# Optimization experiments

Hardware: AMD Instinct MI355X
Metric: run time of the kernel (lower is better)

The kernel has to match this reference:

```python
import jax, jax.numpy as jnp
import numpy as np

EMBED = 512
HEADS = 8
HD = EMBED // HEADS  # 64
LAYERS = 4
VOCAB = 16
SDIM = 3
TDEPTH = 8
BATCH = 2
SEQ = 1024
FF = 4 * EMBED
EPS = 1e-6      # fast-transformers CausalLinearAttention eps
LN_EPS = 1e-5   # torch LayerNorm default


def layer_norm(x, g, b):
    m = jnp.mean(x, axis=-1, keepdims=True)
    v = jnp.mean((x - m) ** 2, axis=-1, keepdims=True)
    return (x - m) * jax.lax.rsqrt(v + LN_EPS) * g + b


def setup_inputs() -> dict:
    key = jax.random.key(0)
    ks = iter(jax.random.split(key, 64))
    def nrm(shape, scale=0.02):
        return jax.random.normal(next(ks), shape, jnp.float32) * scale
    inp = {}
    inp['value'] = jax.random.randint(next(ks), (BATCH, SEQ), 0, VOCAB + 1)
    inp['depth'] = jax.random.randint(next(ks), (BATCH, SEQ), 0, TDEPTH + 1)
    inp['pos'] = jax.random.randint(next(ks), (SDIM, BATCH, SEQ), 0, 2 ** TDEPTH + 1)
    inp['sos'] = jax.random.normal(next(ks), (EMBED,), jnp.float32)
    # embeddings with padding_idx=0 -> zero row 0
    inp['tok_emb'] = nrm((VOCAB + 1, EMBED), 1.0).at[0].set(0.0)
    inp['depth_emb'] = nrm((TDEPTH + 1, EMBED), 1.0).at[0].set(0.0)
    inp['spatial_emb'] = nrm((SDIM, 2 ** TDEPTH + 1, EMBED), 1.0).at[:, 0].set(0.0)
    # per-layer stacked params (weights stored [in, out])
    for nm in ('Wq', 'Wk', 'Wv', 'Wo'):
        inp[nm] = nrm((LAYERS, EMBED, EMBED))
    for nm in ('bq', 'bk', 'bv', 'bo'):
        inp[nm] = jnp.zeros((LAYERS, EMBED), jnp.float32)
    inp['ln1_g'] = jnp.ones((LAYERS, EMBED), jnp.float32)
    inp['ln1_b'] = jnp.zeros((LAYERS, EMBED), jnp.float32)
    inp['ln2_g'] = jnp.ones((LAYERS, EMBED), jnp.float32)
    inp['ln2_b'] = jnp.zeros((LAYERS, EMBED), jnp.float32)
    inp['W1'] = nrm((LAYERS, EMBED, FF))
    inp['b1'] = jnp.zeros((LAYERS, FF), jnp.float32)
    inp['W2'] = nrm((LAYERS, FF, EMBED))
    inp['b2'] = jnp.zeros((LAYERS, EMBED), jnp.float32)
    inp['lnf_g'] = jnp.ones((EMBED,), jnp.float32)
    inp['lnf_b'] = jnp.zeros((EMBED,), jnp.float32)
    inp['Wh'] = nrm((EMBED, VOCAB + 1))
    return inp


def reference(value, depth, pos, sos, tok_emb, depth_emb, spatial_emb,
              Wq, bq, Wk, bk, Wv, bv, Wo, bo,
              ln1_g, ln1_b, ln2_g, ln2_b, W1, b1, W2, b2,
              lnf_g, lnf_b, Wh):
    N, S = value.shape
    # embedding sum
    x = tok_emb[value] + depth_emb[depth]
    for a in range(SDIM):
        x = x + spatial_emb[a][pos[a]]
    # shift right, prepend SOS
    x = jnp.concatenate([jnp.broadcast_to(sos, (N, 1, EMBED)), x[:, :-1, :]], axis=1)
    kmask = (value != 0).astype(x.dtype)  # (N,S) length mask applied to keys
    for i in range(LAYERS):
        # causal-linear attention (elu+1 feature map)
        q = jax.nn.elu((x @ Wq[i] + bq[i]).reshape(N, S, HEADS, HD)) + 1.0
        k = jax.nn.elu((x @ Wk[i] + bk[i]).reshape(N, S, HEADS, HD)) + 1.0
        v = (x @ Wv[i] + bv[i]).reshape(N, S, HEADS, HD)
        k = k * kmask[:, :, None, None]
        kv = jnp.cumsum(jnp.einsum('nshd,nshm->nshdm', k, v), axis=1)  # prefix K^T V state
        num = jnp.einsum('nshd,nshdm->nshm', q, kv)
        z = 1.0 / (jnp.einsum('nshd,nshd->nsh', q, jnp.cumsum(k, axis=1)) + EPS)
        attn = (num * z[..., None]).reshape(N, S, EMBED) @ Wo[i] + bo[i]
        # post-norm transformer block (fast-transformers TransformerEncoderLayer)
        x = layer_norm(x + attn, ln1_g[i], ln1_b[i])
        y = jax.nn.gelu(x @ W1[i] + b1[i], approximate=False) @ W2[i] + b2[i]
        x = layer_norm(x + y, ln2_g[i], ln2_b[i])
    x = layer_norm(x, lnf_g, lnf_b)  # encoder final norm
    return x @ Wh  # (N, S, num_vocab+1)
```

## Files before the change

### kernel.cpp

```cpp
#include <hip/hip_runtime.h>
#include <math.h>

#define EMB 512
#define SEQL 1024
#define NBATCH 2
#define NHEAD 8
#define FFDIM 2048
#define NLAYER 4
#define NROWS (NBATCH*SEQL)
#define CHUNK 128
#define NCH (SEQL/CHUNK)
#define QSTR 1536
#define LN_EPS_F 1e-5f
#define ATT_EPS_F 1e-6f

typedef __bf16 bf16x8 __attribute__((ext_vector_type(8)));
typedef float f32x4 __attribute__((ext_vector_type(4)));

__device__ __forceinline__ unsigned short f2bf(float f) {
    unsigned int u = __float_as_uint(f);
    u += 0x7FFFu + ((u >> 16) & 1u);
    return (unsigned short)(u >> 16);
}
__device__ __forceinline__ float bf2f(unsigned short x) {
    return __uint_as_float(((unsigned int)x) << 16);
}
__device__ __forceinline__ void gl_lds16(const unsigned short* g, unsigned short* l) {
    __builtin_amdgcn_global_load_lds(
        (__attribute__((address_space(1))) void*)const_cast<unsigned short*>(g),
        (__attribute__((address_space(3))) void*)l, 16, 0, 0);
}

__global__ void k_embed(const int* __restrict__ value, const int* __restrict__ depth,
                        const int* __restrict__ pos, const float* __restrict__ sos,
                        const float* __restrict__ tok, const float* __restrict__ dep,
                        const float* __restrict__ spa, float* __restrict__ X,
                        unsigned short* __restrict__ Xb) {
    int row = blockIdx.x;
    int n = row / SEQL, s = row % SEQL;
    int e = threadIdx.x * 4;
    float4 o;
    if (s == 0) {
        o = *(const float4*)(sos + e);
    } else {
        int sp = s - 1;
        int tv = value[n*SEQL + sp];
        int dv = depth[n*SEQL + sp];
        float4 a = *(const float4*)(tok + (size_t)tv*EMB + e);
        float4 b = *(const float4*)(dep + (size_t)dv*EMB + e);
        o.x = a.x+b.x; o.y = a.y+b.y; o.z = a.z+b.z; o.w = a.w+b.w;
#pragma unroll
        for (int ax = 0; ax < 3; ++ax) {
            int p = pos[((size_t)ax*NBATCH + n)*SEQL + sp];
            float4 c = *(const float4*)(spa + ((size_t)ax*257 + p)*EMB + e);
            o.x += c.x; o.y += c.y; o.z += c.z; o.w += c.w;
        }
    }
    *(float4*)(X + (size_t)row*EMB + e) = o;
    ushort4 ob; ob.x = f2bf(o.x); ob.y = f2bf(o.y); ob.z = f2bf(o.z); ob.w = f2bf(o.w);
    *(ushort4*)(Xb + (size_t)row*EMB + e) = ob;
}

__global__ __launch_bounds__(256) void k_wconv(
        const float* __restrict__ Wq0, const float* __restrict__ Wk0, const float* __restrict__ Wv0,
        const float* __restrict__ Wo0, const float* __restrict__ W10, const float* __restrict__ W20,
        const float* __restrict__ bq0, const float* __restrict__ bk0, const float* __restrict__ bv0,
        unsigned short* __restrict__ wAll, float* __restrict__ bqkv) {
    int idx = blockIdx.x*256 + threadIdx.x;
    if (idx >= 1572864) {
        int t = idx - 1572864;
        if (t < 6144) {
            int L = t / 1536, c = t % 1536;
            float v = (c < 512) ? bq0[L*512 + c] : (c < 1024) ? bk0[L*512 + c - 512] : bv0[L*512 + c - 1024];
            bqkv[L*1536 + c] = v;
        }
        return;
    }
    int L = idx / 393216;
    int t0 = idx % 393216;
    const float* Wq = Wq0 + (size_t)L*EMB*EMB;
    const float* Wk = Wk0 + (size_t)L*EMB*EMB;
    const float* Wv = Wv0 + (size_t)L*EMB*EMB;
    const float* Wo = Wo0 + (size_t)L*EMB*EMB;
    const float* W1 = W10 + (size_t)L*EMB*FFDIM;
    const float* W2 = W20 + (size_t)L*FFDIM*EMB;
    unsigned short* lay = wAll + (size_t)L*3145728;
    unsigned short* qkvT = lay;
    unsigned short* woT  = lay + 786432;
    unsigned short* w1T  = lay + 1048576;
    unsigned short* w2T  = lay + 2097152;

    const float* src; unsigned short* dst; size_t soff; size_t doff;
    if (t0 < 131072) {
        int sub = t0 >> 15, t = t0 & 32767;
        int kb = t >> 9, n = t & 511;
        src = (sub == 0) ? Wq : (sub == 1) ? Wk : (sub == 2) ? Wv : Wo;
        soff = (size_t)kb*8*512 + n;
        if (sub < 3) { dst = qkvT; doff = ((size_t)kb*1536 + sub*512 + n)*8; }
        else         { dst = woT;  doff = ((size_t)kb*512 + n)*8; }
        unsigned int p[4];
#pragma unroll
        for (int t2 = 0; t2 < 4; ++t2) {
            unsigned int lo = f2bf(src[soff + (size_t)(2*t2)*512]);
            unsigned int hi = f2bf(src[soff + (size_t)(2*t2+1)*512]);
            p[t2] = lo | (hi << 16);
        }
        *(uint4*)(dst + doff) = make_uint4(p[0], p[1], p[2], p[3]);
    } else if (t0 < 262144) {
        int t = t0 - 131072;
        int kb = t >> 11, n = t & 2047;
        soff = (size_t)kb*8*2048 + n;
        doff = ((size_t)kb*2048 + n)*8;
        unsigned int p[4];
#pragma unroll
        for (int t2 = 0; t2 < 4; ++t2) {
            unsigned int lo = f2bf(W1[soff + (size_t)(2*t2)*2048]);
            unsigned int hi = f2bf(W1[soff + (size_t)(2*t2+1)*2048]);
            p[t2] = lo | (hi << 16);
        }
        *(uint4*)(w1T + doff) = make_uint4(p[0], p[1], p[2], p[3]);
    } else {
        int t = t0 - 262144;
        int kb = t >> 9, n = t & 511;
        soff = (size_t)kb*8*512 + n;
        doff = ((size_t)kb*512 + n)*8;
        unsigned int p[4];
#pragma unroll
        for (int t2 = 0; t2 < 4; ++t2) {
            unsigned int lo = f2bf(W2[soff + (size_t)(2*t2)*512]);
            unsigned int hi = f2bf(W2[soff + (size_t)(2*t2+1)*512]);
            p[t2] = lo | (hi << 16);
        }
        *(uint4*)(w2T + doff) = make_uint4(p[0], p[1], p[2], p[3]);
    }
}

template<int BM, int BN, int WR, int WC, int ACT>
__global__ __launch_bounds__(WR*WC*64) void k_mgemm(
        const unsigned short* __restrict__ A, const unsigned short* __restrict__ Wt,
        const float* __restrict__ bias, const int* __restrict__ maskv,
        float* __restrict__ Cf, unsigned short* __restrict__ Cb,
        int N, int K, int lda, int ldc) {
    constexpr int THREADS = WR*WC*64;
    constexpr int WM = BM/WR, WN = BN/WC;
    constexpr int FM = WM/16, FN = WN/16;
    __shared__ __align__(16) unsigned short As[BM*32];
    __shared__ __align__(16) unsigned short Bs[BN*32];
    int tid = threadIdx.x;
    int lane = tid & 63;
    int l15 = lane & 15, lg = lane >> 4;
    int wid = tid >> 6;
    int wm = (wid / WC) * WM, wn = (wid % WC) * WN;
    int bm = blockIdx.y * BM, bn = blockIdx.x * BN;

    f32x4 acc[FM][FN] = {};

    int a_off = (wm + l15)*32 + lg*8;
    int b_off = lg*BN*8 + (wn + l15)*8;

    for (int k0 = 0; k0 < K; k0 += 32) {
#pragma unroll
        for (int i = 0; i < BM*4/THREADS; ++i) {
            int s = tid + i*THREADS;
            int m = s >> 2, kq = s & 3;
            gl_lds16(A + (size_t)(bm + m)*lda + k0 + kq*8, &As[s*8]);
        }
#pragma unroll
        for (int i = 0; i < BN*4/THREADS; ++i) {
            int s = tid + i*THREADS;
            int kb = s / BN, n = s - kb*BN;
            gl_lds16(Wt + ((size_t)(k0/8 + kb)*N + bn + n)*8, &Bs[s*8]);
        }
        __syncthreads();
        bf16x8 af[FM], bfr[FN];
#pragma unroll
        for (int mi = 0; mi < FM; ++mi) af[mi] = *(const bf16x8*)&As[a_off + mi*512];
#pragma unroll
        for (int ni = 0; ni < FN; ++ni) bfr[ni] = *(const bf16x8*)&Bs[b_off + ni*128];
#pragma unroll
        for (int mi = 0; mi < FM; ++mi)
#pragma unroll
            for (int ni = 0; ni < FN; ++ni)
                acc[mi][ni] = __builtin_amdgcn_mfma_f32_16x16x32_bf16(af[mi], bfr[ni], acc[mi][ni], 0, 0, 0);
        __syncthreads();
    }

    int r0 = bm + wm + lg*4;
    int c0 = bn + wn + l15;
#pragma unroll
    for (int mi = 0; mi < FM; ++mi) {
#pragma unroll
        for (int ni = 0; ni < FN; ++ni) {
            int col = c0 + ni*16;
#pragma unroll
            for (int j = 0; j < 4; ++j) {
                int row = r0 + mi*16 + j;
                float c = acc[mi][ni][j] + bias[col];
                if (ACT == 4) {
                    int reg = col >> 9;
                    if (reg == 0) { c = (c > 0.f) ? c + 1.f : expf(c); }
                    else if (reg == 1) { c = (c > 0.f) ? c + 1.f : expf(c); c *= (maskv[row] != 0) ? 1.f : 0.f; }
                    Cb[(size_t)row*ldc + col] = f2bf(c);
                } else if (ACT == 3) {
                    c = 0.5f * c * (1.f + erff(c * 0.70710678118654752f));
                    Cb[(size_t)row*ldc + col] = f2bf(c);
                } else {
                    Cf[(size_t)row*ldc + col] = c;
                }
            }
        }
    }
}

__global__ __launch_bounds__(256) void k_cpart(
        const unsigned short* __restrict__ QKVb, float* __restrict__ Mpart, float* __restrict__ Upart) {
    int b = blockIdx.x;
    int c = b % NCH, h = (b / NCH) % NHEAD, n = b / (NCH * NHEAD);
    const unsigned short* Kp = QKVb + (size_t)(n*SEQL + c*CHUNK)*QSTR + 512 + h*64;
    const unsigned short* Vp = Kp + 512;
    __shared__ float Ks[8][64], Vs[8][64];
    int tid = threadIdx.x;
    int dk = tid >> 2, dv0 = (tid & 3) * 16;
    int lr = tid >> 5, lc = (tid & 31) * 2;
    float acc[16] = {};
    float uacc = 0.f;
    for (int s0 = 0; s0 < CHUNK; s0 += 8) {
        ushort2 k2 = *(const ushort2*)(Kp + (size_t)(s0 + lr)*QSTR + lc);
        ushort2 v2 = *(const ushort2*)(Vp + (size_t)(s0 + lr)*QSTR + lc);
        Ks[lr][lc] = bf2f(k2.x); Ks[lr][lc+1] = bf2f(k2.y);
        Vs[lr][lc] = bf2f(v2.x); Vs[lr][lc+1] = bf2f(v2.y);
        __syncthreads();
#pragma unroll
        for (int ss = 0; ss < 8; ++ss) {
            float kk = Ks[ss][dk];
#pragma unroll
            for (int j = 0; j < 16; ++j) acc[j] += kk * Vs[ss][dv0 + j];
        }
        if (tid < 64) {
#pragma unroll
            for (int ss = 0; ss < 8; ++ss) uacc += Ks[ss][tid];
        }
        __syncthreads();
    }
    size_t base = ((size_t)(n*NHEAD + h)*NCH + c) * 4096;
#pragma unroll
    for (int j = 0; j < 16; ++j) Mpart[base + (size_t)dk*64 + dv0 + j] = acc[j];
    if (tid < 64) Upart[((size_t)(n*NHEAD + h)*NCH + c)*64 + tid] = uacc;
}

__global__ __launch_bounds__(512) void k_cattend(
        const unsigned short* __restrict__ QKVb, const float* __restrict__ Mpart,
        const float* __restrict__ Upart, unsigned short* __restrict__ Ab) {
    int b = blockIdx.x;
    int c = b % NCH, h = (b / NCH) % NHEAD, n = b / (NCH * NHEAD);
    int nh = n*NHEAD + h;
    int tid = threadIdx.x;
    int wid = tid >> 6, lane = tid & 63;
    int l15 = lane & 15, lg = lane >> 4;
    __shared__ __align__(16) unsigned short Vt[64*200];
    __shared__ __align__(16) unsigned short St[11264];
    __shared__ float wf[64];
    int rowbase = n*SEQL + c*CHUNK;

    {
        int j = tid & 127, vd0 = (tid >> 7) * 16;
        const unsigned short* vp = QKVb + (size_t)(rowbase + j)*QSTR + 1024 + h*64 + vd0;
        uint4 u0 = *(const uint4*)vp;
        uint4 u1 = *(const uint4*)(vp + 8);
        const unsigned short* e0 = (const unsigned short*)&u0;
        const unsigned short* e1 = (const unsigned short*)&u1;
#pragma unroll
        for (int t = 0; t < 8; ++t) Vt[(vd0 + t)*200 + j] = e0[t];
#pragma unroll
        for (int t = 0; t < 8; ++t) Vt[(vd0 + 8 + t)*200 + j] = e1[t];
    }
    {
        int d = tid & 63, vd0 = (tid >> 6) * 8;
        float pr[8] = {};
        for (int cc = 0; cc < c; ++cc) {
            const float* pp = Mpart + ((size_t)nh*NCH + cc)*4096 + (size_t)d*64 + vd0;
            float4 p0 = *(const float4*)pp;
            float4 p1 = *(const float4*)(pp + 4);
            pr[0]+=p0.x; pr[1]+=p0.y; pr[2]+=p0.z; pr[3]+=p0.w;
            pr[4]+=p1.x; pr[5]+=p1.y; pr[6]+=p1.z; pr[7]+=p1.w;
        }
#pragma unroll
        for (int t = 0; t < 8; ++t) Vt[(vd0 + t)*200 + 128 + d] = f2bf(pr[t]);
    }
    if (tid < 64) {
        float u = 0.f;
        for (int cc = 0; cc < c; ++cc) u += Upart[((size_t)nh*NCH + cc)*64 + tid];
        wf[tid] = u;
    }

    int r0 = wid * 16;
    int koff = lg * 8;
    const unsigned short* qp = QKVb + (size_t)(rowbase + r0 + l15)*QSTR + h*64 + koff;
    uint4 uq0 = *(const uint4*)qp;
    uint4 uq1 = *(const uint4*)(qp + 32);
    bf16x8 aq0 = *(bf16x8*)&uq0;
    bf16x8 aq1 = *(bf16x8*)&uq1;

    int nact = (wid & ~1) + 2;
    int sstr_ = 32*((wid >> 1) + 1) + 8;
    int p_ = wid >> 1;
    int sig = p_*(p_+1) + (wid & 1)*(p_+1);
    int stoff_ = 128*wid + 512*sig;

    float rsum[4] = {0.f, 0.f, 0.f, 0.f};
    for (int nt = 0; nt < nact; ++nt) {
        int j0 = nt*16;
        const unsigned short* kp = QKVb + (size_t)(rowbase + j0 + l15)*QSTR + 512 + h*64 + koff;
        uint4 uk0 = *(const uint4*)kp;
        uint4 uk1 = *(const uint4*)(kp + 32);
        f32x4 s = {0.f, 0.f, 0.f, 0.f};
        s = __builtin_amdgcn_mfma_f32_16x16x32_bf16(aq0, *(bf16x8*)&uk0, s, 0, 0, 0);
        s = __builtin_amdgcn_mfma_f32_16x16x32_bf16(aq1, *(bf16x8*)&uk1, s, 0, 0, 0);
        int jcol = j0 + l15;
#pragma unroll
        for (int r = 0; r < 4; ++r) {
            int irow = r0 + lg*4 + r;
            float sv = (jcol <= irow) ? s[r] : 0.f;
            rsum[r] += sv;
            St[stoff_ + (lg*4 + r)*sstr_ + jcol] = f2bf(sv);
        }
    }
    __syncthreads();

    float qw = 0.f;
    const unsigned short* q0e = (const unsigned short*)&uq0;
    const unsigned short* q1e = (const unsigned short*)&uq1;
#pragma unroll
    for (int jj = 0; jj < 8; ++jj) {
        qw += bf2f(q0e[jj]) * wf[koff + jj];
        qw += bf2f(q1e[jj]) * wf[32 + koff + jj];
    }
    qw += __shfl_xor(qw, 16);
    qw += __shfl_xor(qw, 32);

    f32x4 o[4] = {};
    int nkr = (wid >> 1) + 1;
    for (int ks = 0; ks < nkr; ++ks) {
        bf16x8 as = *(bf16x8*)&St[stoff_ + l15*sstr_ + ks*32 + koff];
#pragma unroll
        for (int nt = 0; nt < 4; ++nt) {
            bf16x8 bv = *(bf16x8*)&Vt[(nt*16 + l15)*200 + ks*32 + koff];
            o[nt] = __builtin_amdgcn_mfma_f32_16x16x32_bf16(as, bv, o[nt], 0, 0, 0);
        }
    }
#pragma unroll
    for (int kk = 0; kk < 2; ++kk) {
        bf16x8 as = kk ? aq1 : aq0;
#pragma unroll
        for (int nt = 0; nt < 4; ++nt) {
            bf16x8 bv = *(bf16x8*)&Vt[(nt*16 + l15)*200 + 128 + kk*32 + koff];
            o[nt] = __builtin_amdgcn_mfma_f32_16x16x32_bf16(as, bv, o[nt], 0, 0, 0);
        }
    }

#pragma unroll
    for (int r = 0; r < 4; ++r) {
        float v = rsum[r];
        v += __shfl_xor(v, 1); v += __shfl_xor(v, 2);
        v += __shfl_xor(v, 4); v += __shfl_xor(v, 8);
        rsum[r] = v;
    }
#pragma unroll
    for (int r = 0; r < 4; ++r) {
        float qwr = __shfl(qw, lg*4 + r);
        float z = 1.f / (rsum[r] + qwr + ATT_EPS_F);
        int orow = rowbase + r0 + lg*4 + r;
        unsigned short* op = Ab + (size_t)orow*EMB + h*64 + l15;
#pragma unroll
        for (int nt = 0; nt < 4; ++nt)
            op[nt*16] = f2bf(o[nt][r] * z);
    }
}

__global__ __launch_bounds__(256) void k_ln(
        const float* __restrict__ X, const float* __restrict__ R,
        const float* __restrict__ g, const float* __restrict__ bb,
        float* __restrict__ Y, unsigned short* __restrict__ Yb) {
    int row = blockIdx.x, tid = threadIdx.x;
    float2 v = *(const float2*)(X + (size_t)row*EMB + tid*2);
    {
        float2 r = *(const float2*)(R + (size_t)row*EMB + tid*2);
        v.x += r.x; v.y += r.y;
    }
    float s = v.x + v.y, ss = v.x*v.x + v.y*v.y;
#pragma unroll
    for (int off = 32; off; off >>= 1) {
        s  += __shfl_down(s, off);
        ss += __shfl_down(ss, off);
    }
    __shared__ float sb[4], ssb[4];
    int wid = tid >> 6, lane = tid & 63;
    if (!lane) { sb[wid] = s; ssb[wid] = ss; }
    __syncthreads();
    float tot  = sb[0] + sb[1] + sb[2] + sb[3];
    float tots = ssb[0] + ssb[1] + ssb[2] + ssb[3];
    float mean = tot * (1.f/EMB);
    float var  = tots * (1.f/EMB) - mean*mean;
    float inv  = rsqrtf(var + LN_EPS_F);
    int e = tid*2;
    float2 o;
    o.x = (v.x - mean)*inv*g[e]   + bb[e];
    o.y = (v.y - mean)*inv*g[e+1] + bb[e+1];
    *(float2*)(Y + (size_t)row*EMB + e) = o;
    ushort2 ob; ob.x = f2bf(o.x); ob.y = f2bf(o.y);
    *(ushort2*)(Yb + (size_t)row*EMB + e) = ob;
}

__global__ __launch_bounds__(256) void k_lnhead(
        const float* __restrict__ X, const float* __restrict__ g, const float* __restrict__ bb,
        const float* __restrict__ Wh, float* __restrict__ out) {
    __shared__ float ys[8][512];
    __shared__ float whs[512*17];
    int tid = threadIdx.x;
    for (int i = tid; i < 512*17; i += 256) whs[i] = Wh[i];

    int row = tid >> 5, l32 = tid & 31;
    int rg = blockIdx.x * 8 + row;
    const float* xr = X + (size_t)rg*EMB + l32*16;
    float v[16];
    float s = 0.f, ss = 0.f;
#pragma unroll
    for (int i = 0; i < 4; ++i) {
        float4 a = *(const float4*)(xr + i*4);
        v[i*4+0]=a.x; v[i*4+1]=a.y; v[i*4+2]=a.z; v[i*4+3]=a.w;
        s += a.x+a.y+a.z+a.w;
        ss += a.x*a.x+a.y*a.y+a.z*a.z+a.w*a.w;
    }
#pragma unroll
    for (int off = 1; off < 32; off <<= 1) { s += __shfl_xor(s, off); ss += __shfl_xor(ss, off); }
    float mean = s * (1.f/EMB);
    float var  = ss * (1.f/EMB) - mean*mean;
    float inv  = rsqrtf(var + LN_EPS_F);
    int c0 = l32*16;
#pragma unroll
    for (int i = 0; i < 16; ++i) {
        float y = (v[i] - mean)*inv*g[c0+i] + bb[c0+i];
        ys[row][c0+i] = y;
    }
    __syncthreads();

    float part[17];
#pragma unroll
    for (int cc = 0; cc < 17; ++cc) part[cc] = 0.f;
    for (int kk = 0; kk < 16; ++kk) {
        int k = c0 + kk;
        float yv = ys[row][k];
#pragma unroll
        for (int cc = 0; cc < 17; ++cc) part[cc] += yv * whs[k*17 + cc];
    }
#pragma unroll
    for (int cc = 0; cc < 17; ++cc) {
        float pv = part[cc];
#pragma unroll
        for (int off = 1; off < 32; off <<= 1) pv += __shfl_xor(pv, off);
        if (l32 == 0) out[(size_t)rg*17 + cc] = pv;
    }
}

extern "C" void kernel_launch(void* const* d_in, const int* in_sizes, int n_in,
                              void* d_out, int out_size, void* d_ws, size_t ws_size,
                              hipStream_t stream) {
    (void)in_sizes; (void)n_in; (void)out_size; (void)ws_size;
    const int*   value = (const int*)d_in[0];
    const int*   depth = (const int*)d_in[1];
    const int*   pos   = (const int*)d_in[2];
    const float* sos   = (const float*)d_in[3];
    const float* tok   = (const float*)d_in[4];
    const float* dep   = (const float*)d_in[5];
    const float* spa   = (const float*)d_in[6];
    const float* Wq0   = (const float*)d_in[7];
    const float* Wk0   = (const float*)d_in[8];
    const float* Wv0   = (const float*)d_in[9];
    const float* Wo0   = (const float*)d_in[10];
    const float* bq0   = (const float*)d_in[11];
    const float* bk0   = (const float*)d_in[12];
    const float* bv0   = (const float*)d_in[13];
    const float* bo0   = (const float*)d_in[14];
    const float* ln1g  = (const float*)d_in[15];
    const float* ln1b  = (const float*)d_in[16];
    const float* ln2g  = (const float*)d_in[17];
    const float* ln2b  = (const float*)d_in[18];
    const float* W10   = (const float*)d_in[19];
    const float* b10   = (const float*)d_in[20];
    const float* W20   = (const float*)d_in[21];
    const float* b20   = (const float*)d_in[22];
    const float* lnfg  = (const float*)d_in[23];
    const float* lnfb  = (const float*)d_in[24];
    const float* Wh    = (const float*)d_in[25];
    float* out = (float*)d_out;
    float* ws  = (float*)d_ws;

    float*          X     = ws;
    unsigned short* Xb    = (unsigned short*)(ws + 1048576);
    unsigned short* QKVb  = (unsigned short*)(ws + 1572864);
    unsigned short* Ab    = (unsigned short*)(ws + 3145728);
    unsigned short* Hb    = (unsigned short*)(ws + 1572864);
    float*          Mpart = ws + 3670016;
    float*          Upart = ws + 4194304;
    float*          AO    = ws + 4202496;
    float*          bqkv  = ws + 5251072;
    unsigned short* wAll  = (unsigned short*)(ws + 5257216);

    k_embed<<<NROWS, 128, 0, stream>>>(value, depth, pos, sos, tok, dep, spa, X, Xb);
    k_wconv<<<6168, 256, 0, stream>>>(Wq0, Wk0, Wv0, Wo0, W10, W20, bq0, bk0, bv0, wAll, bqkv);

    for (int L = 0; L < NLAYER; ++L) {
        unsigned short* lay  = wAll + (size_t)L*3145728;
        unsigned short* qkvT = lay;
        unsigned short* woT  = lay + 786432;
        unsigned short* w1T  = lay + 1048576;
        unsigned short* w2T  = lay + 2097152;

        k_mgemm<128,128,4,2,4><<<dim3(12,16), 512, 0, stream>>>(
            Xb, qkvT, bqkv + L*1536, value, nullptr, QKVb, 1536, 512, 512, 1536);

        k_cpart<<<NBATCH*NHEAD*NCH, 256, 0, stream>>>(QKVb, Mpart, Upart);
        k_cattend<<<NBATCH*NHEAD*NCH, 512, 0, stream>>>(QKVb, Mpart, Upart, Ab);

        k_mgemm<64,64,2,2,0><<<dim3(8,32), 256, 0, stream>>>(
            Ab, woT, bo0 + (size_t)L*EMB, nullptr, AO, nullptr, 512, 512, 512, 512);
        k_ln<<<NROWS, 256, 0, stream>>>(X, AO, ln1g + (size_t)L*EMB, ln1b + (size_t)L*EMB, X, Xb);

        k_mgemm<128,128,4,2,3><<<dim3(16,16), 512, 0, stream>>>(
            Xb, w1T, b10 + (size_t)L*FFDIM, nullptr, nullptr, Hb, 2048, 512, 512, 2048);
        k_mgemm<64,64,2,2,0><<<dim3(8,32), 256, 0, stream>>>(
            Hb, w2T, b20 + (size_t)L*EMB, nullptr, AO, nullptr, 512, 2048, 2048, 512);
        k_ln<<<NROWS, 256, 0, stream>>>(X, AO, ln2g + (size_t)L*EMB, ln2b + (size_t)L*EMB, X, Xb);
    }
    k_lnhead<<<NROWS/8, 256, 0, stream>>>(X, lnfg, lnfb, Wh, out);
}
```

Measured before the change: 507.1 us.

## Split-K the narrow GEMMs and reduce partials in LayerNorm; shrink wide GEMM tiles

The Wo and W2 projections (N=512) now use split-K over a grid z-dimension: 2 slices for Wo and 4 for W2. Each slice writes its fp32 partial result to a separate buffer, and the following LayerNorm kernel sums the partials while adding the residual. The QKV and W1 GEMMs move from 128x128 tiles on 512 threads to 64x128 tiles on 256 threads, which doubles the block count. Both changes target low block counts on a many-CU GPU, at the cost of extra partial-buffer traffic and a larger workspace.

```diff
diff --git a/kernel.cpp b/kernel.cpp
--- a/kernel.cpp
+++ b/kernel.cpp
@@ -135,7 +135,7 @@
     }
 }
 
-template<int BM, int BN, int WR, int WC, int ACT>
+template<int BM, int BN, int WR, int WC, int ACT, int KS>
 __global__ __launch_bounds__(WR*WC*64) void k_mgemm(
         const unsigned short* __restrict__ A, const unsigned short* __restrict__ Wt,
         const float* __restrict__ bias, const int* __restrict__ maskv,
@@ -152,13 +152,16 @@
     int wid = tid >> 6;
     int wm = (wid / WC) * WM, wn = (wid % WC) * WN;
     int bm = blockIdx.y * BM, bn = blockIdx.x * BN;
+    int kz = blockIdx.z;
+    int ksl = K / KS;
+    int kbeg = kz * ksl, kend = kbeg + ksl;
 
     f32x4 acc[FM][FN] = {};
 
     int a_off = (wm + l15)*32 + lg*8;
     int b_off = lg*BN*8 + (wn + l15)*8;
 
-    for (int k0 = 0; k0 < K; k0 += 32) {
+    for (int k0 = kbeg; k0 < kend; k0 += 32) {
 #pragma unroll
         for (int i = 0; i < BM*4/THREADS; ++i) {
             int s = tid + i*THREADS;
@@ -187,6 +190,7 @@
 
     int r0 = bm + wm + lg*4;
     int c0 = bn + wn + l15;
+    float* Cfz = Cf + (size_t)kz * 1048576;
 #pragma unroll
     for (int mi = 0; mi < FM; ++mi) {
 #pragma unroll
@@ -195,7 +199,8 @@
 #pragma unroll
             for (int j = 0; j < 4; ++j) {
                 int row = r0 + mi*16 + j;
-                float c = acc[mi][ni][j] + bias[col];
+                float c = acc[mi][ni][j];
+                if (KS == 1 || kz == 0) c += bias[col];
                 if (ACT == 4) {
                     int reg = col >> 9;
                     if (reg == 0) { c = (c > 0.f) ? c + 1.f : expf(c); }
@@ -205,7 +210,7 @@
                     c = 0.5f * c * (1.f + erff(c * 0.70710678118654752f));
                     Cb[(size_t)row*ldc + col] = f2bf(c);
                 } else {
-                    Cf[(size_t)row*ldc + col] = c;
+                    Cfz[(size_t)row*ldc + col] = c;
                 }
             }
         }
@@ -378,13 +383,13 @@
 }
 
 __global__ __launch_bounds__(256) void k_ln(
-        const float* __restrict__ X, const float* __restrict__ R,
+        const float* __restrict__ X, const float* __restrict__ R, int nsl,
         const float* __restrict__ g, const float* __restrict__ bb,
         float* __restrict__ Y, unsigned short* __restrict__ Yb) {
     int row = blockIdx.x, tid = threadIdx.x;
     float2 v = *(const float2*)(X + (size_t)row*EMB + tid*2);
-    {
-        float2 r = *(const float2*)(R + (size_t)row*EMB + tid*2);
+    for (int z = 0; z < nsl; ++z) {
+        float2 r = *(const float2*)(R + (size_t)z*1048576 + (size_t)row*EMB + tid*2);
         v.x += r.x; v.y += r.y;
     }
     float s = v.x + v.y, ss = v.x*v.x + v.y*v.y;
@@ -503,8 +508,8 @@
     float*          Mpart = ws + 3670016;
     float*          Upart = ws + 4194304;
     float*          AO    = ws + 4202496;
-    float*          bqkv  = ws + 5251072;
-    unsigned short* wAll  = (unsigned short*)(ws + 5257216);
+    float*          bqkv  = ws + 8396800;
+    unsigned short* wAll  = (unsigned short*)(ws + 8402944);
 
     k_embed<<<NROWS, 128, 0, stream>>>(value, depth, pos, sos, tok, dep, spa, X, Xb);
     k_wconv<<<6168, 256, 0, stream>>>(Wq0, Wk0, Wv0, Wo0, W10, W20, bq0, bk0, bv0, wAll, bqkv);
@@ -516,21 +521,22 @@
         unsigned short* w1T  = lay + 1048576;
         unsigned short* w2T  = lay + 2097152;
 
-        k_mgemm<128,128,4,2,4><<<dim3(12,16), 512, 0, stream>>>(
+        k_mgemm<64,128,2,2,4,1><<<dim3(12,32), 256, 0, stream>>>(
             Xb, qkvT, bqkv + L*1536, value, nullptr, QKVb, 1536, 512, 512, 1536);
 
         k_cpart<<<NBATCH*NHEAD*NCH, 256, 0, stream>>>(QKVb, Mpart, Upart);
         k_cattend<<<NBATCH*NHEAD*NCH, 512, 0, stream>>>(QKVb, Mpart, Upart, Ab);
 
-        k_mgemm<64,64,2,2,0><<<dim3(8,32), 256, 0, stream>>>(
+        k_mgemm<64,64,2,2,0,2><<<dim3(8,32,2), 256, 0, stream>>>(
             Ab, woT, bo0 + (size_t)L*EMB, nullptr, AO, nullptr, 512, 512, 512, 512);
-        k_ln<<<NROWS, 256, 0, stream>>>(X, AO, ln1g + (size_t)L*EMB, ln1b + (size_t)L*EMB, X, Xb);
-
-        k_mgemm<128,128,4,2,3><<<dim3(16,16), 512, 0, stream>>>(
+        k_ln<<<NROWS, 256, 0, stream>>>(X, AO, 2, ln1g + (size_t)L*EMB, ln1b + (size_t)L*EMB, X, Xb);
+
+        k_mgemm<64,128,2,2,3,1><<<dim3(16,32), 256, 0, stream>>>(
             Xb, w1T, b10 + (size_t)L*FFDIM, nullptr, nullptr, Hb, 2048, 512, 512, 2048);
-        k_mgemm<64,64,2,2,0><<<dim3(8,32), 256, 0, stream>>>(
+
+        k_mgemm<64,64,2,2,0,4><<<dim3(8,32,4), 256, 0, stream>>>(
             Hb, w2T, b20 + (size_t)L*EMB, nullptr, AO, nullptr, 512, 2048, 2048, 512);
-        k_ln<<<NROWS, 256, 0, stream>>>(X, AO, ln2g + (size_t)L*EMB, ln2b + (size_t)L*EMB, X, Xb);
+        k_ln<<<NROWS, 256, 0, stream>>>(X, AO, 4, ln2g + (size_t)L*EMB, ln2b + (size_t)L*EMB, X, Xb);
     }
     k_lnhead<<<NROWS/8, 256, 0, stream>>>(X, lnfg, lnfb, Wh, out);
 }
```

Measured after the change: 424.4 us. 16.3% less time.
